# Kernel optimization log

Measured on AMD Instinct MI355X. Metric: run time of the kernel, lower is better.

The kernel has to match this reference:

```python
import jax, jax.numpy as jnp
import numpy as np

B, S, D, H, DK = 8, 1024, 768, 12, 64


def setup_inputs() -> dict:
    key = jax.random.key(0)
    k1, k2, k3, k4, k5 = jax.random.split(key, 5)
    return {
        "x": jax.random.normal(k1, (B, S, D), dtype=jnp.float32),
        "Wq": jax.random.normal(k2, (H, D, DK), dtype=jnp.float32),
        "Wk": jax.random.normal(k3, (H, D, DK), dtype=jnp.float32),
        "Wv": jax.random.normal(k4, (H, D, DK), dtype=jnp.float32),
        "W": jax.random.normal(k5, (D, D), dtype=jnp.float32),
    }


def reference(x, Wq, Wk, Wv, W):
    # Batched equivalent of the per-head SelfAttention loop + concat + W matmul.
    q = jnp.einsum("bsd,hdk->bhsk", x, Wq)  # [B,H,S,DK]
    k = jnp.einsum("bsd,hdk->bhsk", x, Wk)
    v = jnp.einsum("bsd,hdk->bhsk", x, Wv)
    scale = 1.0 / jnp.sqrt(jnp.asarray(DK, dtype=x.dtype))
    scores = jnp.einsum("bhsk,bhtk->bhst", q, k) * scale  # [B,H,S,S]
    attn = jax.nn.softmax(scores, axis=-1)
    z = jnp.einsum("bhst,bhtk->bhsk", attn, v)  # [B,H,S,DK]
    # concat heads along last dim: [B,S,H*DK]
    z = jnp.transpose(z, (0, 2, 1, 3)).reshape(x.shape[0], x.shape[1], H * DK)
    return jnp.matmul(z, W)  # [B,S,D]
```

## Files before the change

kernel.cpp:

```cpp
#include <hip/hip_runtime.h>

#define Bv 8
#define Sv 1024
#define Dv 768
#define Hv 12
#define DKv 64
#define Mv (Bv*Sv)
#define NQKV (3*Hv*DKv)
#define NQK (2*Hv*DKv)

typedef __attribute__((ext_vector_type(8))) short short8;
typedef __attribute__((ext_vector_type(4))) short short4v;
typedef __attribute__((ext_vector_type(4))) float f32x4;

__device__ __forceinline__ short f2bf(float f) {
    unsigned u = __builtin_bit_cast(unsigned, f);
    u += 0x7fffu + ((u >> 16) & 1u);
    return (short)(u >> 16);
}
__device__ __forceinline__ float bf2f(short h) {
    return __builtin_bit_cast(float, (unsigned)(unsigned short)h << 16);
}

__device__ __forceinline__ f32x4 mfma16(short8 a, short8 b, f32x4 c) {
    return __builtin_amdgcn_mfma_f32_16x16x32_bf16(a, b, c, 0, 0, 0);
}

__device__ __forceinline__ void gload16(const short* g, const short* l) {
    __builtin_amdgcn_global_load_lds(
        (const __attribute__((address_space(1))) unsigned int*)g,
        (__attribute__((address_space(3))) unsigned int*)(short*)l, 16, 0, 0);
}

__global__ __launch_bounds__(256) void prep_kernel(const float* __restrict__ x,
                                                   const float* __restrict__ Wq,
                                                   const float* __restrict__ Wk,
                                                   const float* __restrict__ Wv,
                                                   const float* __restrict__ W,
                                                   short* __restrict__ xh, short* __restrict__ xl,
                                                   short* __restrict__ Wh, short* __restrict__ Wl,
                                                   short* __restrict__ W2T) {
    __shared__ float lds[64][65];
    int bid = blockIdx.x;
    int t = threadIdx.x;
    if (bid < 3072) {
        int idx = bid * 256 + t;
        const float4* f = (const float4*)x + (size_t)idx * 2;
        float4 a = f[0], b = f[1];
        float v[8] = {a.x,a.y,a.z,a.w,b.x,b.y,b.z,b.w};
        short8 oh, ol;
#pragma unroll
        for (int k = 0; k < 8; k++) {
            short hi = f2bf(v[k]);
            oh[k] = hi;
            ol[k] = f2bf(v[k] - bf2f(hi));
        }
        *((short8*)xh + idx) = oh;
        *((short8*)xl + idx) = ol;
    } else if (bid < 3504) {
        int idx = bid - 3072;
        int dt = idx % 12, h = (idx / 12) % 12, p = idx / 144;
        const float* S = (p == 0 ? Wq : (p == 1 ? Wk : Wv)) + (size_t)h * Dv * DKv;
        float sc = (p == 0) ? 0.125f : 1.0f;
        int d0 = dt * 64;
#pragma unroll
        for (int i = 0; i < 4; i++) {
            int v = t + i * 256;
            int r = v >> 4, c4 = v & 15;
            float4 f = *(const float4*)&S[(size_t)(d0 + r) * DKv + c4 * 4];
            lds[r][c4*4+0] = f.x; lds[r][c4*4+1] = f.y; lds[r][c4*4+2] = f.z; lds[r][c4*4+3] = f.w;
        }
        __syncthreads();
#pragma unroll
        for (int i = 0; i < 2; i++) {
            int v = t + i * 256;
            int kk = v >> 3, dl0 = (v & 7) * 8;
            short8 oh, ol;
#pragma unroll
            for (int k = 0; k < 8; k++) {
                float f = lds[dl0 + k][kk] * sc;
                short hi = f2bf(f);
                oh[k] = hi;
                ol[k] = f2bf(f - bf2f(hi));
            }
            size_t base = (size_t)(p*768 + h*64 + kk) * Dv + d0 + dl0;
            *(short8*)&Wh[base] = oh;
            if (p < 2) *(short8*)&Wl[base] = ol;
        }
    } else {
        int idx = bid - 3504;
        int c0 = (idx % 12) * 64, r0 = (idx / 12) * 64;
#pragma unroll
        for (int i = 0; i < 4; i++) {
            int v = t + i * 256;
            int r = v >> 4, c4 = v & 15;
            float4 f = *(const float4*)&W[(size_t)(r0 + r) * Dv + c0 + c4 * 4];
            lds[r][c4*4+0] = f.x; lds[r][c4*4+1] = f.y; lds[r][c4*4+2] = f.z; lds[r][c4*4+3] = f.w;
        }
        __syncthreads();
#pragma unroll
        for (int i = 0; i < 2; i++) {
            int v = t + i * 256;
            int oc = v >> 3, rl0 = (v & 7) * 8;
            short8 o;
#pragma unroll
            for (int k = 0; k < 8; k++) o[k] = f2bf(lds[rl0 + k][oc]);
            *(short8*)&W2T[(size_t)(c0 + oc) * Dv + r0 + rl0] = o;
        }
    }
}

__device__ __forceinline__ void swz_xy(int n, int& xbl, int& ybl) {
    int cx = n & 7, k = n >> 3;
    ybl = cx + 8 * (k & 7);
    xbl = k >> 3;
}

__global__ __launch_bounds__(256, 4) void gemm1_kernel(const short* __restrict__ xh,
                                                       const short* __restrict__ xl,
                                                       const short* __restrict__ Wh,
                                                       const short* __restrict__ Wl,
                                                       short* __restrict__ QKVh,
                                                       short* __restrict__ QKVl,
                                                       short* __restrict__ Vt) {
    int xbl, ybl;
    swz_xy(blockIdx.x, xbl, ybl);
    int m0 = ybl * 128, n0 = xbl * 128;
    bool isv = (n0 >= NQK);
    int KT = isv ? 24 : 72;
    __shared__ __align__(16) short lA[2][4096];
    __shared__ __align__(16) short lB[2][4096];
    int tid = threadIdx.x, lane = tid & 63, w = tid >> 6;
    int wr = w >> 1, wc = w & 1;
    int li = lane & 15, g = lane >> 4;
    f32x4 zero = {0.f, 0.f, 0.f, 0.f};
    f32x4 acc[4][4];
#pragma unroll
    for (int i = 0; i < 4; i++)
#pragma unroll
        for (int j = 0; j < 4; j++) acc[i][j] = zero;

    int e0 = tid * 8;
    int sr0 = e0 >> 5;
    int sc0 = ((e0 >> 3) & 3) ^ ((sr0 >> 1) & 3);
    int sr1 = sr0 + 64;
    int sc1 = ((e0 >> 3) & 3) ^ ((sr1 >> 1) & 3);

    auto stage = [&](int t, int buf) {
        int seg = (t >= 48) ? 2 : (t >= 24 ? 1 : 0);
        int kk = (t - seg * 24) * 32;
        const short* Ab = (seg == 2) ? xl : xh;
        const short* Bb = (seg == 1) ? Wl : Wh;
        gload16(Ab + (size_t)(m0 + sr0) * Dv + kk + sc0 * 8, &lA[buf][w * 512]);
        gload16(Bb + (size_t)(n0 + sr0) * Dv + kk + sc0 * 8, &lB[buf][w * 512]);
        gload16(Ab + (size_t)(m0 + sr1) * Dv + kk + sc1 * 8, &lA[buf][2048 + w * 512]);
        gload16(Bb + (size_t)(n0 + sr1) * Dv + kk + sc1 * 8, &lB[buf][2048 + w * 512]);
    };

    stage(0, 0);
    stage(1, 1);

    for (int t = 0; t < KT; t++) {
        int cur = t & 1;
        if (t + 1 < KT) asm volatile("s_waitcnt vmcnt(4)" ::: "memory");
        else            asm volatile("s_waitcnt vmcnt(0)" ::: "memory");
        __builtin_amdgcn_s_barrier();
        __builtin_amdgcn_sched_barrier(0);
        short8 a[4], bb[4];
#pragma unroll
        for (int mi = 0; mi < 4; mi++) {
            int row = wr*64 + mi*16 + li;
            a[mi] = *(const short8*)&lA[cur][row * 32 + ((g ^ ((row >> 1) & 3)) << 3)];
        }
#pragma unroll
        for (int ni = 0; ni < 4; ni++) {
            int row = wc*64 + ni*16 + li;
            bb[ni] = *(const short8*)&lB[cur][row * 32 + ((g ^ ((row >> 1) & 3)) << 3)];
        }
#pragma unroll
        for (int mi = 0; mi < 4; mi++)
#pragma unroll
            for (int ni = 0; ni < 4; ni++)
                acc[mi][ni] = mfma16(a[mi], bb[ni], acc[mi][ni]);
        __builtin_amdgcn_sched_barrier(0);
        __builtin_amdgcn_s_barrier();
        __builtin_amdgcn_sched_barrier(0);
        if (t + 2 < KT) stage(t + 2, cur);
    }
    if (isv) {
#pragma unroll
        for (int mi = 0; mi < 4; mi++)
#pragma unroll
            for (int ni = 0; ni < 4; ni++) {
                int vcol = n0 + wc*64 + ni*16 + li - NQK;
                int h = vcol >> 6, dk = vcol & 63;
                int row0 = m0 + wr*64 + mi*16 + g*4;
                int b = row0 >> 10, s0 = row0 & 1023;
                short4v v4;
                v4[0] = f2bf(acc[mi][ni][0]); v4[1] = f2bf(acc[mi][ni][1]);
                v4[2] = f2bf(acc[mi][ni][2]); v4[3] = f2bf(acc[mi][ni][3]);
                *(short4v*)&Vt[(size_t)((b*Hv + h)*64 + dk) * Sv + s0] = v4;
            }
    } else {
#pragma unroll
        for (int mi = 0; mi < 4; mi++)
#pragma unroll
            for (int ni = 0; ni < 4; ni++)
#pragma unroll
                for (int j = 0; j < 4; j++) {
                    int row = m0 + wr*64 + mi*16 + g*4 + j;
                    int col = n0 + wc*64 + ni*16 + li;
                    float v = acc[mi][ni][j];
                    short hi = f2bf(v);
                    QKVh[(size_t)row * NQKV + col] = hi;
                    QKVl[(size_t)row * NQK + col] = f2bf(v - bf2f(hi));
                }
    }
}

__global__ __launch_bounds__(256, 4) void gemm2_kernel(const short* __restrict__ A,
                                                       const short* __restrict__ Bt,
                                                       float* __restrict__ C) {
    int xbl, ybl;
    swz_xy(blockIdx.x, xbl, ybl);
    int m0 = ybl * 128, n0 = xbl * 128;
    __shared__ __align__(16) short lA[2][4096];
    __shared__ __align__(16) short lB[2][4096];
    int tid = threadIdx.x, lane = tid & 63, w = tid >> 6;
    int wr = w >> 1, wc = w & 1;
    int li = lane & 15, g = lane >> 4;
    f32x4 zero = {0.f, 0.f, 0.f, 0.f};
    f32x4 acc[4][4];
#pragma unroll
    for (int i = 0; i < 4; i++)
#pragma unroll
        for (int j = 0; j < 4; j++) acc[i][j] = zero;

    int e0 = tid * 8;
    int sr0 = e0 >> 5;
    int sc0 = ((e0 >> 3) & 3) ^ ((sr0 >> 1) & 3);
    int sr1 = sr0 + 64;
    int sc1 = ((e0 >> 3) & 3) ^ ((sr1 >> 1) & 3);

    auto stage = [&](int t, int buf) {
        int kk = t * 32;
        gload16(A  + (size_t)(m0 + sr0) * Dv + kk + sc0 * 8, &lA[buf][w * 512]);
        gload16(Bt + (size_t)(n0 + sr0) * Dv + kk + sc0 * 8, &lB[buf][w * 512]);
        gload16(A  + (size_t)(m0 + sr1) * Dv + kk + sc1 * 8, &lA[buf][2048 + w * 512]);
        gload16(Bt + (size_t)(n0 + sr1) * Dv + kk + sc1 * 8, &lB[buf][2048 + w * 512]);
    };

    stage(0, 0);
    stage(1, 1);

    for (int t = 0; t < 24; t++) {
        int cur = t & 1;
        if (t + 1 < 24) asm volatile("s_waitcnt vmcnt(4)" ::: "memory");
        else            asm volatile("s_waitcnt vmcnt(0)" ::: "memory");
        __builtin_amdgcn_s_barrier();
        __builtin_amdgcn_sched_barrier(0);
        short8 a[4], bb[4];
#pragma unroll
        for (int mi = 0; mi < 4; mi++) {
            int row = wr*64 + mi*16 + li;
            a[mi] = *(const short8*)&lA[cur][row * 32 + ((g ^ ((row >> 1) & 3)) << 3)];
        }
#pragma unroll
        for (int ni = 0; ni < 4; ni++) {
            int row = wc*64 + ni*16 + li;
            bb[ni] = *(const short8*)&lB[cur][row * 32 + ((g ^ ((row >> 1) & 3)) << 3)];
        }
#pragma unroll
        for (int mi = 0; mi < 4; mi++)
#pragma unroll
            for (int ni = 0; ni < 4; ni++)
                acc[mi][ni] = mfma16(a[mi], bb[ni], acc[mi][ni]);
        __builtin_amdgcn_sched_barrier(0);
        __builtin_amdgcn_s_barrier();
        __builtin_amdgcn_sched_barrier(0);
        if (t + 2 < 24) stage(t + 2, cur);
    }
#pragma unroll
    for (int mi = 0; mi < 4; mi++)
#pragma unroll
        for (int ni = 0; ni < 4; ni++)
#pragma unroll
            for (int j = 0; j < 4; j++) {
                int row = m0 + wr*64 + mi*16 + g*4 + j;
                int col = n0 + wc*64 + ni*16 + li;
                C[(size_t)row * Dv + col] = acc[mi][ni][j];
            }
}

__global__ __launch_bounds__(512, 6) void attn_kernel(const short* __restrict__ QKVh,
                                                      const short* __restrict__ QKVl,
                                                      const short* __restrict__ Vt,
                                                      short* __restrict__ Z) {
    int n = blockIdx.x;
    int j2 = n >> 3;
    int bh = (n & 7) + 8 * (j2 >> 3);
    int qb = j2 & 7;
    int b = bh / Hv, h = bh % Hv;
    int tid = threadIdx.x, lane = tid & 63, w = tid >> 6;
    int li = lane & 15, g = lane >> 4;

    __shared__ __align__(16) short Kh[64 * 64];
    __shared__ __align__(16) short Kl[64 * 64];
    __shared__ __align__(16) short Vs[64 * 64];
    __shared__ __align__(16) short P[8][1024];
    char* Pw = (char*)&P[w][0];
    const char* Khc = (const char*)Kh;
    const char* Klc = (const char*)Kl;
    const char* Vsc = (const char*)Vs;

    int qr0 = qb * 128 + w * 16;
    const short* qhr = QKVh + (size_t)(b*Sv + qr0 + li) * NQKV + h * DKv;
    const short* qlr = QKVl + (size_t)(b*Sv + qr0 + li) * NQK  + h * DKv;
    short8 qh0 = *(const short8*)(qhr + g * 8);
    short8 qh1 = *(const short8*)(qhr + 32 + g * 8);
    short8 ql0 = *(const short8*)(qlr + g * 8);
    short8 ql1 = *(const short8*)(qlr + 32 + g * 8);

    const short* Khb = QKVh + (size_t)(b*Sv) * NQKV + Hv*DKv + h*DKv;
    const short* Klb = QKVl + (size_t)(b*Sv) * NQK  + Hv*DKv + h*DKv;
    const short* Vbase = Vt + (size_t)(bh * 64) * Sv;

    int srow = w * 8 + (lane >> 3);
    int scs  = (lane & 7) ^ (srow & 7);

    float mm = -1e30f, ll = 0.f;
    f32x4 zero = {0.f, 0.f, 0.f, 0.f};
    f32x4 acc[4];
#pragma unroll
    for (int ni = 0; ni < 4; ni++) acc[ni] = zero;

    for (int t = 0; t < 16; t++) {
        int t0 = t * 64;
        gload16(Khb + (size_t)(t0 + srow) * NQKV + scs * 8, &Kh[w * 512]);
        gload16(Klb + (size_t)(t0 + srow) * NQK  + scs * 8, &Kl[w * 512]);
        gload16(Vbase + (size_t)srow * Sv + t0 + scs * 8,   &Vs[w * 512]);
        __syncthreads();

        f32x4 s[4];
#pragma unroll
        for (int tn = 0; tn < 4; tn++) {
            int row = tn * 16 + li;
            int rb = row * 128, rs = (row & 7) << 4;
            short8 kh0 = *(const short8*)(Khc + rb + ((g << 4) ^ rs));
            short8 kh1 = *(const short8*)(Khc + rb + ((64 + (g << 4)) ^ rs));
            short8 kl0 = *(const short8*)(Klc + rb + ((g << 4) ^ rs));
            short8 kl1 = *(const short8*)(Klc + rb + ((64 + (g << 4)) ^ rs));
            f32x4 z = mfma16(kh0, qh0, zero);
            z = mfma16(kh1, qh1, z);
            z = mfma16(kl0, qh0, z);
            z = mfma16(kl1, qh1, z);
            z = mfma16(kh0, ql0, z);
            z = mfma16(kh1, ql1, z);
            s[tn] = z;
        }
        float rm = s[0][0];
#pragma unroll
        for (int tn = 0; tn < 4; tn++)
#pragma unroll
            for (int jj = 0; jj < 4; jj++) rm = fmaxf(rm, s[tn][jj]);
        rm = fmaxf(rm, __shfl_xor(rm, 16));
        rm = fmaxf(rm, __shfl_xor(rm, 32));
        float mn = fmaxf(mm, rm);
        float sfu = __expf(mm - mn);
        float p[4][4];
        float rs2 = 0.f;
#pragma unroll
        for (int tn = 0; tn < 4; tn++)
#pragma unroll
            for (int jj = 0; jj < 4; jj++) { p[tn][jj] = __expf(s[tn][jj] - mn); rs2 += p[tn][jj]; }
        rs2 += __shfl_xor(rs2, 16);
        rs2 += __shfl_xor(rs2, 32);
        ll = ll * sfu + rs2;
        mm = mn;

        float sfq[4];
#pragma unroll
        for (int jj = 0; jj < 4; jj++) sfq[jj] = __shfl(sfu, g * 4 + jj);
#pragma unroll
        for (int ni = 0; ni < 4; ni++)
#pragma unroll
            for (int jj = 0; jj < 4; jj++) acc[ni][jj] *= sfq[jj];

#pragma unroll
        for (int tn = 0; tn < 4; tn++) {
            unsigned lo, hi;
            asm("v_cvt_pk_bf16_f32 %0, %1, %2" : "=v"(lo) : "v"(p[tn][0]), "v"(p[tn][1]));
            asm("v_cvt_pk_bf16_f32 %0, %1, %2" : "=v"(hi) : "v"(p[tn][2]), "v"(p[tn][3]));
            unsigned long long pk = (unsigned long long)lo | ((unsigned long long)hi << 32);
            int off = (li * 128 + tn * 32 + g * 8) ^ ((li & 7) << 4);
            *(unsigned long long*)(Pw + off) = pk;
        }
#pragma unroll
        for (int kt = 0; kt < 2; kt++) {
            int roff = (li * 128 + kt * 64 + g * 16) ^ ((li & 7) << 4);
            short8 ap = *(const short8*)(Pw + roff);
#pragma unroll
            for (int ni = 0; ni < 4; ni++) {
                int dk = ni * 16 + li;
                int vb = dk * 128 + ((((kt * 4 + g) << 4)) ^ ((dk & 7) << 4));
                short8 bv = *(const short8*)(Vsc + vb);
                acc[ni] = mfma16(ap, bv, acc[ni]);
            }
        }
        __syncthreads();
    }
    float inv = 1.f / ll;
    float invq[4];
#pragma unroll
    for (int jj = 0; jj < 4; jj++) invq[jj] = __shfl(inv, g * 4 + jj);
#pragma unroll
    for (int ni = 0; ni < 4; ni++)
#pragma unroll
        for (int jj = 0; jj < 4; jj++) {
            int row = b*Sv + qr0 + g*4 + jj;
            int col = h*DKv + ni*16 + li;
            Z[(size_t)row * Dv + col] = f2bf(acc[ni][jj] * invq[jj]);
        }
}

extern "C" void kernel_launch(void* const* d_in, const int* in_sizes, int n_in,
                              void* d_out, int out_size, void* d_ws, size_t ws_size,
                              hipStream_t stream) {
    const float* x  = (const float*)d_in[0];
    const float* Wq = (const float*)d_in[1];
    const float* Wk = (const float*)d_in[2];
    const float* Wv = (const float*)d_in[3];
    const float* W  = (const float*)d_in[4];
    float* out = (float*)d_out;

    short* xh   = (short*)d_ws;
    short* xl   = xh   + (size_t)Mv * Dv;
    short* Wh   = xl   + (size_t)Mv * Dv;
    short* Wl   = Wh   + (size_t)NQKV * Dv;
    short* W2T  = Wl   + (size_t)NQKV * Dv;
    short* QKVh = W2T  + (size_t)Dv * Dv;
    short* QKVl = QKVh + (size_t)Mv * NQKV;
    short* Vt   = QKVl + (size_t)Mv * NQK;
    short* Zb   = Vt   + (size_t)Bv*Hv*DKv * Sv;

    prep_kernel<<<dim3(3648), 256, 0, stream>>>(x, Wq, Wk, Wv, W, xh, xl, Wh, Wl, W2T);
    gemm1_kernel<<<dim3((NQKV/128) * (Mv/128)), 256, 0, stream>>>(xh, xl, Wh, Wl, QKVh, QKVl, Vt);
    attn_kernel<<<dim3(768), 512, 0, stream>>>(QKVh, QKVl, Vt, Zb);
    gemm2_kernel<<<dim3((Dv/128) * (Mv/128)), 256, 0, stream>>>(Zb, W2T, out);
}
```

Before: 192.6 us.

## Load GEMM A operands directly to registers and split QK/V projection kernels

```diff
diff --git a/kernel.cpp b/kernel.cpp
--- a/kernel.cpp
+++ b/kernel.cpp
@@ -30,6 +30,9 @@
     __builtin_amdgcn_global_load_lds(
         (const __attribute__((address_space(1))) unsigned int*)g,
         (__attribute__((address_space(3))) unsigned int*)(short*)l, 16, 0, 0);
+}
+__device__ __forceinline__ void gloadreg(short8& d, const short* p) {
+    asm volatile("global_load_dwordx4 %0, %1, off" : "=v"(d) : "v"(p) : "memory");
 }
 
 __global__ __launch_bounds__(256) void prep_kernel(const float* __restrict__ x,
@@ -116,170 +119,159 @@
     xbl = k >> 3;
 }
 
-__global__ __launch_bounds__(256, 4) void gemm1_kernel(const short* __restrict__ xh,
-                                                       const short* __restrict__ xl,
-                                                       const short* __restrict__ Wh,
-                                                       const short* __restrict__ Wl,
-                                                       short* __restrict__ QKVh,
-                                                       short* __restrict__ QKVl,
-                                                       short* __restrict__ Vt) {
+#define GEMM_PRE()                                                              \
+    __shared__ __align__(16) short lB[2][4096];                                 \
+    int tid = threadIdx.x, lane = tid & 63, w = tid >> 6;                       \
+    int wr = w >> 1, wc = w & 1;                                                \
+    int li = lane & 15, g = lane >> 4;                                          \
+    f32x4 zero = {0.f, 0.f, 0.f, 0.f};                                          \
+    f32x4 acc[4][4];                                                            \
+    _Pragma("unroll") for (int i = 0; i < 4; i++)                               \
+        _Pragma("unroll") for (int j = 0; j < 4; j++) acc[i][j] = zero;         \
+    int e0 = tid * 8;                                                           \
+    int sr0 = e0 >> 5;                                                          \
+    int sc0 = ((e0 >> 3) & 3) ^ ((sr0 >> 1) & 3);                               \
+    int sr1 = sr0 + 64;                                                         \
+    int sc1 = ((e0 >> 3) & 3) ^ ((sr1 >> 1) & 3);                               \
+    size_t arow[4];                                                             \
+    _Pragma("unroll") for (int mi = 0; mi < 4; mi++)                            \
+        arow[mi] = (size_t)(m0 + wr*64 + mi*16 + li) * Dv + g * 8;              \
+    short8 a0[4], a1[4], bb[4];
+
+#define GEMM_STEP(T, KT, ACUR, BUF)                                             \
+    {                                                                           \
+        if ((T) < (KT) - 1) asm volatile("s_waitcnt vmcnt(6)" ::: "memory");    \
+        else                asm volatile("s_waitcnt vmcnt(0)" ::: "memory");    \
+        __builtin_amdgcn_s_barrier();                                           \
+        __builtin_amdgcn_sched_barrier(0);                                      \
+        _Pragma("unroll") for (int ni = 0; ni < 4; ni++) {                      \
+            int row = wc*64 + ni*16 + li;                                       \
+            bb[ni] = *(const short8*)&lB[BUF][row * 32 + ((g ^ ((row >> 1) & 3)) << 3)]; \
+        }                                                                       \
+        _Pragma("unroll") for (int mi = 0; mi < 4; mi++)                        \
+            _Pragma("unroll") for (int ni = 0; ni < 4; ni++)                    \
+                acc[mi][ni] = mfma16(ACUR[mi], bb[ni], acc[mi][ni]);            \
+        __builtin_amdgcn_sched_barrier(0);                                      \
+        __builtin_amdgcn_s_barrier();                                           \
+        __builtin_amdgcn_sched_barrier(0);                                      \
+        if ((T) + 2 < (KT)) { ISSUE((T) + 2, ACUR, BUF); }                      \
+        __builtin_amdgcn_sched_barrier(0);                                      \
+    }
+
+__global__ __launch_bounds__(256, 3) void gemm_qk_kernel(const short* __restrict__ xh,
+                                                         const short* __restrict__ xl,
+                                                         const short* __restrict__ Wh,
+                                                         const short* __restrict__ Wl,
+                                                         short* __restrict__ QKVh,
+                                                         short* __restrict__ QKVl) {
     int xbl, ybl;
     swz_xy(blockIdx.x, xbl, ybl);
     int m0 = ybl * 128, n0 = xbl * 128;
-    bool isv = (n0 >= NQK);
-    int KT = isv ? 24 : 72;
-    __shared__ __align__(16) short lA[2][4096];
-    __shared__ __align__(16) short lB[2][4096];
-    int tid = threadIdx.x, lane = tid & 63, w = tid >> 6;
-    int wr = w >> 1, wc = w & 1;
-    int li = lane & 15, g = lane >> 4;
-    f32x4 zero = {0.f, 0.f, 0.f, 0.f};
-    f32x4 acc[4][4];
-#pragma unroll
-    for (int i = 0; i < 4; i++)
-#pragma unroll
-        for (int j = 0; j < 4; j++) acc[i][j] = zero;
-
-    int e0 = tid * 8;
-    int sr0 = e0 >> 5;
-    int sc0 = ((e0 >> 3) & 3) ^ ((sr0 >> 1) & 3);
-    int sr1 = sr0 + 64;
-    int sc1 = ((e0 >> 3) & 3) ^ ((sr1 >> 1) & 3);
-
-    auto stage = [&](int t, int buf) {
-        int seg = (t >= 48) ? 2 : (t >= 24 ? 1 : 0);
-        int kk = (t - seg * 24) * 32;
-        const short* Ab = (seg == 2) ? xl : xh;
-        const short* Bb = (seg == 1) ? Wl : Wh;
-        gload16(Ab + (size_t)(m0 + sr0) * Dv + kk + sc0 * 8, &lA[buf][w * 512]);
-        gload16(Bb + (size_t)(n0 + sr0) * Dv + kk + sc0 * 8, &lB[buf][w * 512]);
-        gload16(Ab + (size_t)(m0 + sr1) * Dv + kk + sc1 * 8, &lA[buf][2048 + w * 512]);
-        gload16(Bb + (size_t)(n0 + sr1) * Dv + kk + sc1 * 8, &lB[buf][2048 + w * 512]);
-    };
-
-    stage(0, 0);
-    stage(1, 1);
-
-    for (int t = 0; t < KT; t++) {
-        int cur = t & 1;
-        if (t + 1 < KT) asm volatile("s_waitcnt vmcnt(4)" ::: "memory");
-        else            asm volatile("s_waitcnt vmcnt(0)" ::: "memory");
-        __builtin_amdgcn_s_barrier();
-        __builtin_amdgcn_sched_barrier(0);
-        short8 a[4], bb[4];
-#pragma unroll
-        for (int mi = 0; mi < 4; mi++) {
-            int row = wr*64 + mi*16 + li;
-            a[mi] = *(const short8*)&lA[cur][row * 32 + ((g ^ ((row >> 1) & 3)) << 3)];
-        }
+    const int KT = 72;
+    GEMM_PRE();
+
+#define ISSUE(T, ACUR, BUF)                                                     \
+    {                                                                           \
+        int seg = (T) >= 48 ? 2 : ((T) >= 24 ? 1 : 0);                          \
+        int kk = ((T) - seg * 24) * 32;                                         \
+        const short* Ab = (seg == 2) ? xl : xh;                                 \
+        const short* Bb = (seg == 1) ? Wl : Wh;                                 \
+        _Pragma("unroll") for (int mi = 0; mi < 4; mi++)                        \
+            gloadreg(ACUR[mi], Ab + arow[mi] + kk);                             \
+        gload16(Bb + (size_t)(n0 + sr0) * Dv + kk + sc0 * 8, &lB[BUF][w * 512]); \
+        gload16(Bb + (size_t)(n0 + sr1) * Dv + kk + sc1 * 8, &lB[BUF][2048 + w * 512]); \
+    }
+
+    ISSUE(0, a0, 0);
+    ISSUE(1, a1, 1);
+    for (int t = 0; t < KT; t += 2) {
+        GEMM_STEP(t, KT, a0, 0);
+        GEMM_STEP(t + 1, KT, a1, 1);
+    }
+#undef ISSUE
+
+#pragma unroll
+    for (int mi = 0; mi < 4; mi++)
+#pragma unroll
+        for (int ni = 0; ni < 4; ni++)
+#pragma unroll
+            for (int j = 0; j < 4; j++) {
+                int row = m0 + wr*64 + mi*16 + g*4 + j;
+                int col = n0 + wc*64 + ni*16 + li;
+                float v = acc[mi][ni][j];
+                short hi = f2bf(v);
+                QKVh[(size_t)row * NQKV + col] = hi;
+                QKVl[(size_t)row * NQK + col] = f2bf(v - bf2f(hi));
+            }
+}
+
+__global__ __launch_bounds__(256, 3) void gemm_v_kernel(const short* __restrict__ xh,
+                                                        const short* __restrict__ Wh,
+                                                        short* __restrict__ Vt) {
+    int xbl, ybl;
+    swz_xy(blockIdx.x, xbl, ybl);
+    int m0 = ybl * 128, n0 = NQK + xbl * 128;
+    const int KT = 24;
+    GEMM_PRE();
+
+#define ISSUE(T, ACUR, BUF)                                                     \
+    {                                                                           \
+        int kk = (T) * 32;                                                      \
+        _Pragma("unroll") for (int mi = 0; mi < 4; mi++)                        \
+            gloadreg(ACUR[mi], xh + arow[mi] + kk);                             \
+        gload16(Wh + (size_t)(n0 + sr0) * Dv + kk + sc0 * 8, &lB[BUF][w * 512]); \
+        gload16(Wh + (size_t)(n0 + sr1) * Dv + kk + sc1 * 8, &lB[BUF][2048 + w * 512]); \
+    }
+
+    ISSUE(0, a0, 0);
+    ISSUE(1, a1, 1);
+    for (int t = 0; t < KT; t += 2) {
+        GEMM_STEP(t, KT, a0, 0);
+        GEMM_STEP(t + 1, KT, a1, 1);
+    }
+#undef ISSUE
+
+#pragma unroll
+    for (int mi = 0; mi < 4; mi++)
 #pragma unroll
         for (int ni = 0; ni < 4; ni++) {
-            int row = wc*64 + ni*16 + li;
-            bb[ni] = *(const short8*)&lB[cur][row * 32 + ((g ^ ((row >> 1) & 3)) << 3)];
-        }
-#pragma unroll
-        for (int mi = 0; mi < 4; mi++)
-#pragma unroll
-            for (int ni = 0; ni < 4; ni++)
-                acc[mi][ni] = mfma16(a[mi], bb[ni], acc[mi][ni]);
-        __builtin_amdgcn_sched_barrier(0);
-        __builtin_amdgcn_s_barrier();
-        __builtin_amdgcn_sched_barrier(0);
-        if (t + 2 < KT) stage(t + 2, cur);
-    }
-    if (isv) {
-#pragma unroll
-        for (int mi = 0; mi < 4; mi++)
-#pragma unroll
-            for (int ni = 0; ni < 4; ni++) {
-                int vcol = n0 + wc*64 + ni*16 + li - NQK;
-                int h = vcol >> 6, dk = vcol & 63;
-                int row0 = m0 + wr*64 + mi*16 + g*4;
-                int b = row0 >> 10, s0 = row0 & 1023;
-                short4v v4;
-                v4[0] = f2bf(acc[mi][ni][0]); v4[1] = f2bf(acc[mi][ni][1]);
-                v4[2] = f2bf(acc[mi][ni][2]); v4[3] = f2bf(acc[mi][ni][3]);
-                *(short4v*)&Vt[(size_t)((b*Hv + h)*64 + dk) * Sv + s0] = v4;
-            }
-    } else {
-#pragma unroll
-        for (int mi = 0; mi < 4; mi++)
-#pragma unroll
-            for (int ni = 0; ni < 4; ni++)
-#pragma unroll
-                for (int j = 0; j < 4; j++) {
-                    int row = m0 + wr*64 + mi*16 + g*4 + j;
-                    int col = n0 + wc*64 + ni*16 + li;
-                    float v = acc[mi][ni][j];
-                    short hi = f2bf(v);
-                    QKVh[(size_t)row * NQKV + col] = hi;
-                    QKVl[(size_t)row * NQK + col] = f2bf(v - bf2f(hi));
-                }
-    }
-}
-
-__global__ __launch_bounds__(256, 4) void gemm2_kernel(const short* __restrict__ A,
+            int vcol = n0 + wc*64 + ni*16 + li - NQK;
+            int h = vcol >> 6, dk = vcol & 63;
+            int row0 = m0 + wr*64 + mi*16 + g*4;
+            int b = row0 >> 10, s0 = row0 & 1023;
+            short4v v4;
+            v4[0] = f2bf(acc[mi][ni][0]); v4[1] = f2bf(acc[mi][ni][1]);
+            v4[2] = f2bf(acc[mi][ni][2]); v4[3] = f2bf(acc[mi][ni][3]);
+            *(short4v*)&Vt[(size_t)((b*Hv + h)*64 + dk) * Sv + s0] = v4;
+        }
+}
+
+__global__ __launch_bounds__(256, 3) void gemm2_kernel(const short* __restrict__ A,
                                                        const short* __restrict__ Bt,
                                                        float* __restrict__ C) {
     int xbl, ybl;
     swz_xy(blockIdx.x, xbl, ybl);
     int m0 = ybl * 128, n0 = xbl * 128;
-    __shared__ __align__(16) short lA[2][4096];
-    __shared__ __align__(16) short lB[2][4096];
-    int tid = threadIdx.x, lane = tid & 63, w = tid >> 6;
-    int wr = w >> 1, wc = w & 1;
-    int li = lane & 15, g = lane >> 4;
-    f32x4 zero = {0.f, 0.f, 0.f, 0.f};
-    f32x4 acc[4][4];
-#pragma unroll
-    for (int i = 0; i < 4; i++)
-#pragma unroll
-        for (int j = 0; j < 4; j++) acc[i][j] = zero;
-
-    int e0 = tid * 8;
-    int sr0 = e0 >> 5;
-    int sc0 = ((e0 >> 3) & 3) ^ ((sr0 >> 1) & 3);
-    int sr1 = sr0 + 64;
-    int sc1 = ((e0 >> 3) & 3) ^ ((sr1 >> 1) & 3);
-
-    auto stage = [&](int t, int buf) {
-        int kk = t * 32;
-        gload16(A  + (size_t)(m0 + sr0) * Dv + kk + sc0 * 8, &lA[buf][w * 512]);
-        gload16(Bt + (size_t)(n0 + sr0) * Dv + kk + sc0 * 8, &lB[buf][w * 512]);
-        gload16(A  + (size_t)(m0 + sr1) * Dv + kk + sc1 * 8, &lA[buf][2048 + w * 512]);
-        gload16(Bt + (size_t)(n0 + sr1) * Dv + kk + sc1 * 8, &lB[buf][2048 + w * 512]);
-    };
-
-    stage(0, 0);
-    stage(1, 1);
-
-    for (int t = 0; t < 24; t++) {
-        int cur = t & 1;
-        if (t + 1 < 24) asm volatile("s_waitcnt vmcnt(4)" ::: "memory");
-        else            asm volatile("s_waitcnt vmcnt(0)" ::: "memory");
-        __builtin_amdgcn_s_barrier();
-        __builtin_amdgcn_sched_barrier(0);
-        short8 a[4], bb[4];
-#pragma unroll
-        for (int mi = 0; mi < 4; mi++) {
-            int row = wr*64 + mi*16 + li;
-            a[mi] = *(const short8*)&lA[cur][row * 32 + ((g ^ ((row >> 1) & 3)) << 3)];
-        }
-#pragma unroll
-        for (int ni = 0; ni < 4; ni++) {
-            int row = wc*64 + ni*16 + li;
-            bb[ni] = *(const short8*)&lB[cur][row * 32 + ((g ^ ((row >> 1) & 3)) << 3)];
-        }
-#pragma unroll
-        for (int mi = 0; mi < 4; mi++)
-#pragma unroll
-            for (int ni = 0; ni < 4; ni++)
-                acc[mi][ni] = mfma16(a[mi], bb[ni], acc[mi][ni]);
-        __builtin_amdgcn_sched_barrier(0);
-        __builtin_amdgcn_s_barrier();
-        __builtin_amdgcn_sched_barrier(0);
-        if (t + 2 < 24) stage(t + 2, cur);
-    }
+    const int KT = 24;
+    GEMM_PRE();
+
+#define ISSUE(T, ACUR, BUF)                                                     \
+    {                                                                           \
+        int kk = (T) * 32;                                                      \
+        _Pragma("unroll") for (int mi = 0; mi < 4; mi++)                        \
+            gloadreg(ACUR[mi], A + arow[mi] + kk);                              \
+        gload16(Bt + (size_t)(n0 + sr0) * Dv + kk + sc0 * 8, &lB[BUF][w * 512]); \
+        gload16(Bt + (size_t)(n0 + sr1) * Dv + kk + sc1 * 8, &lB[BUF][2048 + w * 512]); \
+    }
+
+    ISSUE(0, a0, 0);
+    ISSUE(1, a1, 1);
+    for (int t = 0; t < KT; t += 2) {
+        GEMM_STEP(t, KT, a0, 0);
+        GEMM_STEP(t + 1, KT, a1, 1);
+    }
+#undef ISSUE
+
 #pragma unroll
     for (int mi = 0; mi < 4; mi++)
 #pragma unroll
@@ -444,7 +436,8 @@
     short* Zb   = Vt   + (size_t)Bv*Hv*DKv * Sv;
 
     prep_kernel<<<dim3(3648), 256, 0, stream>>>(x, Wq, Wk, Wv, W, xh, xl, Wh, Wl, W2T);
-    gemm1_kernel<<<dim3((NQKV/128) * (Mv/128)), 256, 0, stream>>>(xh, xl, Wh, Wl, QKVh, QKVl, Vt);
+    gemm_qk_kernel<<<dim3((NQK/128) * (Mv/128)), 256, 0, stream>>>(xh, xl, Wh, Wl, QKVh, QKVl);
+    gemm_v_kernel<<<dim3((Dv/128) * (Mv/128)), 256, 0, stream>>>(xh, Wh, Vt);
     attn_kernel<<<dim3(768), 512, 0, stream>>>(QKVh, QKVl, Vt, Zb);
     gemm2_kernel<<<dim3((Dv/128) * (Mv/128)), 256, 0, stream>>>(Zb, W2T, out);
 }
```

After: 264.0 us. +37.1%, slower.
